# Performance work log

Hardware: AMD Instinct MI355X
Metric: run time of the kernel (lower is better)

The kernel has to match this reference:

```python
import jax, jax.numpy as jnp
import numpy as np

N_NODES = 10000
N_EDGES = 160000
IN_DIM = 512
HID = 128
HEADS = 8
EMB = 256
NEG_SLOPE = 0.2  # PyG GATConv default


def setup_inputs() -> dict:
    key = jax.random.key(0)
    ks = jax.random.split(key, 12)
    x = jax.random.normal(ks[0], (N_NODES, IN_DIM), dtype=jnp.float32)
    edge_index = jax.random.randint(ks[1], (2, N_EDGES), 0, N_NODES, dtype=jnp.int64)
    s1 = 1.0 / np.sqrt(IN_DIM)
    s2 = 1.0 / np.sqrt(HEADS * HID)
    W1 = jax.random.normal(ks[2], (IN_DIM, HEADS * HID), dtype=jnp.float32) * s1
    a_src1 = jax.random.normal(ks[3], (HEADS, HID), dtype=jnp.float32) * s2
    a_dst1 = jax.random.normal(ks[4], (HEADS, HID), dtype=jnp.float32) * s2
    b1 = jnp.zeros((HEADS * HID,), dtype=jnp.float32)
    W2 = jax.random.normal(ks[5], (HEADS * HID, EMB), dtype=jnp.float32) * s2
    a_src2 = jax.random.normal(ks[6], (1, EMB), dtype=jnp.float32) * (1.0 / np.sqrt(EMB))
    a_dst2 = jax.random.normal(ks[7], (1, EMB), dtype=jnp.float32) * (1.0 / np.sqrt(EMB))
    b2 = jnp.zeros((EMB,), dtype=jnp.float32)
    return {"x": x, "edge_index": edge_index, "W1": W1, "a_src1": a_src1,
            "a_dst1": a_dst1, "b1": b1, "W2": W2, "a_src2": a_src2,
            "a_dst2": a_dst2, "b2": b2}


def gat_layer(h_in, src, dst, W, a_src, a_dst, b, concat, num_nodes):
    """PyG-style GATConv (eval mode, self-loops already in src/dst)."""
    H, C = a_src.shape
    h = (h_in @ W).reshape(num_nodes, H, C)            # [N, H, C]
    alpha_src = jnp.einsum('nhc,hc->nh', h, a_src)      # [N, H]
    alpha_dst = jnp.einsum('nhc,hc->nh', h, a_dst)      # [N, H]
    e = jax.nn.leaky_relu(alpha_src[src] + alpha_dst[dst], NEG_SLOPE)  # [E, H]
    # segment softmax over incoming edges of each destination node
    m = jax.ops.segment_max(e, dst, num_segments=num_nodes)            # [N, H]
    ex = jnp.exp(e - m[dst])
    denom = jax.ops.segment_sum(ex, dst, num_segments=num_nodes)       # [N, H]
    alpha = ex / denom[dst]                                            # [E, H]
    out = jax.ops.segment_sum(h[src] * alpha[:, :, None], dst,
                              num_segments=num_nodes)                  # [N, H, C]
    out = out.reshape(num_nodes, H * C) if concat else out.mean(axis=1)
    return out + b


def reference(x, edge_index, W1, a_src1, a_dst1, b1, W2, a_src2, a_dst2, b2):
    N = x.shape[0]
    loops = jnp.arange(N, dtype=edge_index.dtype)
    src = jnp.concatenate([edge_index[0], loops])
    dst = jnp.concatenate([edge_index[1], loops])
    h = gat_layer(x, src, dst, W1, a_src1, a_dst1, b1, concat=True, num_nodes=N)
    h = jax.nn.elu(h)  # dropout inactive in eval mode
    out = gat_layer(h, src, dst, W2, a_src2, a_dst2, b2, concat=False, num_nodes=N)
    return out
```

## Files before the change

### kernel.cpp

```cpp
#include <hip/hip_runtime.h>
#include <hip/hip_bf16.h>

typedef __attribute__((ext_vector_type(8))) short short8;
typedef __attribute__((ext_vector_type(4))) float floatx4;
typedef __attribute__((ext_vector_type(4))) unsigned short ushort4v;
typedef __attribute__((ext_vector_type(8))) unsigned short ushort8v;

#define NN 10000
#define E0 160000
#define ETOT (E0 + NN)
#define IN_DIM 512
#define HID1 1024
#define EMB 256
#define MPAD 10112
#define LDSS 40

__device__ __forceinline__ float bf2f(unsigned short u) {
    unsigned v = ((unsigned)u) << 16;
    float f;
    __builtin_memcpy(&f, &v, 4);
    return f;
}
__device__ __forceinline__ unsigned short f2bf(float f) {
    unsigned u;
    __builtin_memcpy(&u, &f, 4);
    unsigned lsb = (u >> 16) & 1;
    u += 0x7fff + lsb;
    return (unsigned short)(u >> 16);
}
__device__ __forceinline__ float loadf(const void* p, size_t i, int isf32) {
    if (isf32) return ((const float*)p)[i];
    return bf2f(((const unsigned short*)p)[i]);
}

__global__ void zero_kernel(int* p, int n) {
    int i = blockIdx.x * 256 + threadIdx.x;
    if (i < n) p[i] = 0;
}

__global__ __launch_bounds__(1024) void fdetect_kernel(const unsigned* xw, int* isf32) {
    __shared__ int cnt[1024];
    int t = threadIdx.x;
    int c = 0;
    #pragma unroll
    for (int j = 0; j < 4; ++j) {
        unsigned w = xw[t * 4 + j];
        int ex = (w >> 7) & 0xFF;
        if (ex >= 110 && ex <= 135) c++;
    }
    cnt[t] = c;
    __syncthreads();
    for (int off = 512; off > 0; off >>= 1) {
        if (t < off) cnt[t] += cnt[t + off];
        __syncthreads();
    }
    if (t == 0) *isf32 = (cnt[0] < 2048) ? 1 : 0;
}

__global__ void detect_kernel(const int* ei32, int* flag) {
    int i = blockIdx.x * 256 + threadIdx.x;
    int v = 0;
    int idx = 2 * i + 1;
    if (idx < 2 * E0) v = ei32[idx];
    unsigned long long any = __ballot(v != 0);
    if (any && (threadIdx.x & 63) == 0) atomicOr(flag, 1);
}

__device__ __forceinline__ int load_edge(const void* ei, long long idx, int m32) {
    if (m32) return ((const int*)ei)[idx];
    return (int)(((const long long*)ei)[idx]);
}

__global__ void count_kernel(const void* ei, const int* flag, int* counts) {
    int e = blockIdx.x * 256 + threadIdx.x;
    if (e < E0) {
        int m32 = (*flag != 0);
        int d = load_edge(ei, (long long)E0 + e, m32);
        if (d >= 0 && d < NN) atomicAdd(&counts[d], 1);
    }
}

__global__ __launch_bounds__(1024) void scan_kernel(const int* counts, int* offsets, int* cursor) {
    __shared__ int part[1024];
    int t = threadIdx.x;
    int base = t * 10;
    int local[10];
    int s = 0;
    for (int j = 0; j < 10; ++j) {
        int idx = base + j;
        int v = (idx < NN) ? (counts[idx] + 1) : 0;
        local[j] = v; s += v;
    }
    part[t] = s;
    __syncthreads();
    for (int off = 1; off < 1024; off <<= 1) {
        int v = (t >= off) ? part[t - off] : 0;
        __syncthreads();
        part[t] += v;
        __syncthreads();
    }
    int run = (t == 0) ? 0 : part[t - 1];
    for (int j = 0; j < 10; ++j) {
        int idx = base + j;
        if (idx < NN) { offsets[idx] = run; cursor[idx] = run; run += local[j]; }
    }
    if (t == 1023) offsets[NN] = part[1023];
}

__global__ void scatter_kernel(const void* ei, const int* flag, int* cursor, int* csr_src) {
    int e = blockIdx.x * 256 + threadIdx.x;
    if (e >= ETOT) return;
    int m32 = (*flag != 0);
    int s, d;
    if (e < E0) { s = load_edge(ei, e, m32); d = load_edge(ei, (long long)E0 + e, m32); }
    else { s = d = e - E0; }
    if (s < 0) s = 0; if (s >= NN) s = NN - 1;
    if (d < 0) d = 0; if (d >= NN) d = NN - 1;
    int pos = atomicAdd(&cursor[d], 1);
    if (pos >= 0 && pos < ETOT) csr_src[pos] = s;
}

__global__ void conv_kernel(const void* in, unsigned short* out, int n, const int* isf32) {
    int i = blockIdx.x * 256 + threadIdx.x;
    if (i < n) out[i] = f2bf(loadf(in, i, *isf32));
}

__global__ void convT_kernel(const void* in, unsigned short* out, int R, int C, const int* isf32) {
    int i = blockIdx.x * 256 + threadIdx.x;
    if (i < R * C) {
        int r = i / C, c = i % C;
        out[(size_t)c * R + r] = f2bf(loadf(in, i, *isf32));
    }
}

template<bool OUTBF16>
__global__ __launch_bounds__(256) void gemm_tile(
    const unsigned short* __restrict__ A,
    const unsigned short* __restrict__ Bt,
    void* __restrict__ Cv,
    int N, int K)
{
    __shared__ unsigned short As[128 * LDSS];
    __shared__ unsigned short Bs[128 * LDSS];
    int t = threadIdx.x;
    int wave = t >> 6;
    int lane = t & 63;
    int quad = lane >> 4;
    int l16  = lane & 15;
    int mq = wave & 1, nq = wave >> 1;
    size_t mblk = (size_t)blockIdx.x * 128;
    size_t nblk = (size_t)blockIdx.y * 128;

    int srow = t >> 2;
    int skof = (t & 3) * 8;

    floatx4 acc[4][4];
    #pragma unroll
    for (int i = 0; i < 4; ++i)
        #pragma unroll
        for (int j = 0; j < 4; ++j)
            acc[i][j] = (floatx4){0.f, 0.f, 0.f, 0.f};

    const unsigned short* Ab = A + mblk * K + skof;
    const unsigned short* Bb = Bt + nblk * K + skof;

    for (int kk = 0; kk < K; kk += 32) {
        short8 a0 = *(const short8*)(const void*)(Ab + (size_t)srow * K + kk);
        short8 a1 = *(const short8*)(const void*)(Ab + (size_t)(srow + 64) * K + kk);
        short8 b0 = *(const short8*)(const void*)(Bb + (size_t)srow * K + kk);
        short8 b1 = *(const short8*)(const void*)(Bb + (size_t)(srow + 64) * K + kk);
        __syncthreads();
        *(short8*)(void*)(As + srow * LDSS + skof)        = a0;
        *(short8*)(void*)(As + (srow + 64) * LDSS + skof) = a1;
        *(short8*)(void*)(Bs + srow * LDSS + skof)        = b0;
        *(short8*)(void*)(Bs + (srow + 64) * LDSS + skof) = b1;
        __syncthreads();

        short8 af[4], bf[4];
        #pragma unroll
        for (int i = 0; i < 4; ++i) {
            af[i] = *(const short8*)(const void*)(As + (mq * 64 + i * 16 + l16) * LDSS + quad * 8);
            bf[i] = *(const short8*)(const void*)(Bs + (nq * 64 + i * 16 + l16) * LDSS + quad * 8);
        }
        #pragma unroll
        for (int i = 0; i < 4; ++i)
            #pragma unroll
            for (int j = 0; j < 4; ++j)
                acc[i][j] = __builtin_amdgcn_mfma_f32_16x16x32_bf16(af[i], bf[j], acc[i][j], 0, 0, 0);
    }

    size_t crow0 = mblk + mq * 64 + quad * 4;
    size_t ccol0 = nblk + nq * 64 + l16;
    #pragma unroll
    for (int i = 0; i < 4; ++i) {
        #pragma unroll
        for (int r = 0; r < 4; ++r) {
            size_t row = crow0 + i * 16 + r;
            size_t b = row * N + ccol0;
            #pragma unroll
            for (int j = 0; j < 4; ++j) {
                if (OUTBF16) ((unsigned short*)Cv)[b + j * 16] = f2bf(acc[i][j][r]);
                else         ((float*)Cv)[b + j * 16] = acc[i][j][r];
            }
        }
    }
}

__global__ __launch_bounds__(256) void alpha1_kernel(
    const unsigned short* __restrict__ h1,
    const void* __restrict__ a_src, const void* __restrict__ a_dst,
    const int* __restrict__ isf32,
    float* __restrict__ as1, float* __restrict__ ad1)
{
    int n = blockIdx.x, t = threadIdx.x;
    int f = *isf32;
    ushort4v hv = *(const ushort4v*)(const void*)(h1 + (size_t)n * HID1 + t * 4);
    float ps = 0.f, pd = 0.f;
    #pragma unroll
    for (int i = 0; i < 4; ++i) {
        float h = bf2f(hv[i]);
        ps += h * loadf(a_src, t * 4 + i, f);
        pd += h * loadf(a_dst, t * 4 + i, f);
    }
    __shared__ float rs[256], rdm[256];
    rs[t] = ps; rdm[t] = pd;
    __syncthreads();
    for (int off = 16; off > 0; off >>= 1) {
        if ((t & 31) < off) { rs[t] += rs[t + off]; rdm[t] += rdm[t + off]; }
        __syncthreads();
    }
    if ((t & 31) == 0) {
        int h = t >> 5;
        as1[n * 8 + h] = rs[t];
        ad1[n * 8 + h] = rdm[t];
    }
}

__global__ __launch_bounds__(256) void agg1_kernel(
    const unsigned short* __restrict__ h1, const int* __restrict__ offsets,
    const int* __restrict__ csr_src, const float* __restrict__ as1,
    const float* __restrict__ ad1, const void* __restrict__ b1,
    const int* __restrict__ isf32,
    unsigned short* __restrict__ hmid)
{
    int n = blockIdx.x, t = threadIdx.x;
    int f = *isf32;
    int beg = offsets[n], end = offsets[n + 1];
    if (beg < 0) beg = 0; if (end > ETOT) end = ETOT;
    int g = t >> 7;
    int u = t & 127;
    int c0 = u * 8;
    int hc = u >> 4;
    float ad = ad1[n * 8 + hc];

    float den = 0.f;
    float acc[8];
    #pragma unroll
    for (int j = 0; j < 8; ++j) acc[j] = 0.f;

    for (int i = beg + g; i < end; i += 2) {
        int s = csr_src[i]; s &= 0x7fffffff; if (s >= NN) s = 0;
        float e = as1[s * 8 + hc] + ad;
        e = e > 0.f ? e : 0.2f * e;
        float w = __expf(e);
        den += w;
        ushort8v hv = *(const ushort8v*)(const void*)(h1 + (size_t)s * HID1 + c0);
        #pragma unroll
        for (int j = 0; j < 8; ++j) acc[j] += bf2f(hv[j]) * w;
    }

    __shared__ float accsh[128][8];
    __shared__ float densh[128];
    if (g == 1) {
        #pragma unroll
        for (int j = 0; j < 8; ++j) accsh[u][j] = acc[j];
        densh[u] = den;
    }
    __syncthreads();
    if (g == 0) {
        den += densh[u];
        float rden = 1.0f / fmaxf(den, 1e-30f);
        ushort8v outw;
        #pragma unroll
        for (int j = 0; j < 8; ++j) {
            float v = (acc[j] + accsh[u][j]) * rden + loadf(b1, c0 + j, f);
            v = v > 0.f ? v : (__expf(v) - 1.0f);
            outw[j] = f2bf(v);
        }
        *(ushort8v*)(void*)(hmid + (size_t)n * HID1 + c0) = outw;
    }
}

__global__ __launch_bounds__(256) void alpha2_kernel(
    const unsigned short* __restrict__ h2,
    const void* __restrict__ a_src2, const void* __restrict__ a_dst2,
    const int* __restrict__ isf32,
    float* __restrict__ as2, float* __restrict__ ad2)
{
    int n = blockIdx.x, t = threadIdx.x;
    int f = *isf32;
    float v = bf2f(h2[(size_t)n * EMB + t]);
    float ps = v * loadf(a_src2, t, f);
    float pd = v * loadf(a_dst2, t, f);
    __shared__ float rs[256], rdm[256];
    rs[t] = ps; rdm[t] = pd;
    __syncthreads();
    for (int off = 128; off > 0; off >>= 1) {
        if (t < off) { rs[t] += rs[t + off]; rdm[t] += rdm[t + off]; }
        __syncthreads();
    }
    if (t == 0) { as2[n] = rs[0]; ad2[n] = rdm[0]; }
}

__global__ __launch_bounds__(256) void agg2_kernel(
    const unsigned short* __restrict__ h2, const int* __restrict__ offsets,
    const int* __restrict__ csr_src, const float* __restrict__ as2,
    const float* __restrict__ ad2, const void* __restrict__ b2,
    const int* __restrict__ isf32,
    float* __restrict__ out)
{
    int n = blockIdx.x, t = threadIdx.x;
    int f = *isf32;
    int beg = offsets[n], end = offsets[n + 1];
    if (beg < 0) beg = 0; if (end > ETOT) end = ETOT;
    int g = t >> 6;
    int u = t & 63;
    int c0 = u * 4;
    float adn = ad2[n];

    float den = 0.f;
    float acc[4];
    #pragma unroll
    for (int j = 0; j < 4; ++j) acc[j] = 0.f;

    for (int i = beg + g; i < end; i += 4) {
        int s = csr_src[i]; s &= 0x7fffffff; if (s >= NN) s = 0;
        float e = as2[s] + adn;
        e = e > 0.f ? e : 0.2f * e;
        float w = __expf(e);
        den += w;
        ushort4v hv = *(const ushort4v*)(const void*)(h2 + (size_t)s * EMB + c0);
        #pragma unroll
        for (int j = 0; j < 4; ++j) acc[j] += bf2f(hv[j]) * w;
    }

    __shared__ float accsh[4][64][4];
    __shared__ float densh[4][64];
    #pragma unroll
    for (int j = 0; j < 4; ++j) accsh[g][u][j] = acc[j];
    densh[g][u] = den;
    __syncthreads();
    if (g == 0) {
        float dtot = densh[0][u] + densh[1][u] + densh[2][u] + densh[3][u];
        float rden = 1.0f / fmaxf(dtot, 1e-30f);
        floatx4 o;
        #pragma unroll
        for (int j = 0; j < 4; ++j) {
            float v = (accsh[0][u][j] + accsh[1][u][j] + accsh[2][u][j] + accsh[3][u][j]) * rden;
            o[j] = v + loadf(b2, c0 + j, f);
        }
        *(floatx4*)(void*)(out + (size_t)n * EMB + c0) = o;
    }
}

extern "C" void kernel_launch(void* const* d_in, const int* in_sizes, int n_in,
                              void* d_out, int out_size, void* d_ws, size_t ws_size,
                              hipStream_t stream)
{
    const void* x      = d_in[0];
    const void* edge   = d_in[1];
    const void* W1     = d_in[2];
    const void* a_src1 = d_in[3];
    const void* a_dst1 = d_in[4];
    const void* b1     = d_in[5];
    const void* W2     = d_in[6];
    const void* a_src2 = d_in[7];
    const void* a_dst2 = d_in[8];
    const void* b2     = d_in[9];
    float* out = (float*)d_out;

    char* ws = (char*)d_ws;
    size_t off = 0;
    auto alloc = [&](size_t bytes) -> void* {
        void* p = ws + off;
        off += (bytes + 255) & ~(size_t)255;
        return p;
    };
    int*            counts = (int*)alloc((NN + 2) * 4);
    int*            offs   = (int*)alloc((NN + 1) * 4);
    int*            cursor = (int*)alloc(NN * 4);
    int*            csr    = (int*)alloc((size_t)ETOT * 4);
    float*          as1    = (float*)alloc((size_t)NN * 8 * 4);
    float*          ad1    = (float*)alloc((size_t)NN * 8 * 4);
    float*          as2    = (float*)alloc((size_t)NN * 4);
    float*          ad2    = (float*)alloc((size_t)NN * 4);
    unsigned short* xb     = (unsigned short*)alloc((size_t)MPAD * IN_DIM * 2);
    unsigned short* W1t    = (unsigned short*)alloc((size_t)IN_DIM * HID1 * 2);
    unsigned short* W2t    = (unsigned short*)alloc((size_t)HID1 * EMB * 2);
    unsigned short* h1b    = (unsigned short*)alloc((size_t)MPAD * HID1 * 2);
    unsigned short* hmid   = (unsigned short*)alloc((size_t)MPAD * HID1 * 2);
    unsigned short* h2b    = (unsigned short*)alloc((size_t)MPAD * EMB * 2);
    int* eflag = counts + NN;
    int* isf32 = counts + NN + 1;

    zero_kernel<<<(NN + 2 + 255) / 256, 256, 0, stream>>>(counts, NN + 2);
    fdetect_kernel<<<1, 1024, 0, stream>>>((const unsigned*)x, isf32);
    detect_kernel<<<(E0 + 255) / 256, 256, 0, stream>>>((const int*)edge, eflag);

    count_kernel<<<(E0 + 255) / 256, 256, 0, stream>>>(edge, eflag, counts);
    scan_kernel<<<1, 1024, 0, stream>>>(counts, offs, cursor);
    scatter_kernel<<<(ETOT + 255) / 256, 256, 0, stream>>>(edge, eflag, cursor, csr);

    conv_kernel<<<(NN * IN_DIM + 255) / 256, 256, 0, stream>>>(x, xb, NN * IN_DIM, isf32);
    convT_kernel<<<(IN_DIM * HID1 + 255) / 256, 256, 0, stream>>>(W1, W1t, IN_DIM, HID1, isf32);
    convT_kernel<<<(HID1 * EMB + 255) / 256, 256, 0, stream>>>(W2, W2t, HID1, EMB, isf32);

    dim3 g1(MPAD / 128, HID1 / 128);
    gemm_tile<true><<<g1, 256, 0, stream>>>(xb, W1t, h1b, HID1, IN_DIM);

    alpha1_kernel<<<NN, 256, 0, stream>>>(h1b, a_src1, a_dst1, isf32, as1, ad1);
    agg1_kernel<<<NN, 256, 0, stream>>>(h1b, offs, csr, as1, ad1, b1, isf32, hmid);

    dim3 g2(MPAD / 128, EMB / 128);
    gemm_tile<true><<<g2, 256, 0, stream>>>(hmid, W2t, h2b, EMB, HID1);

    alpha2_kernel<<<NN, 256, 0, stream>>>(h2b, a_src2, a_dst2, isf32, as2, ad2);
    agg2_kernel<<<NN, 256, 0, stream>>>(h2b, offs, csr, as2, ad2, b2, isf32, out);
}
```

Before: 325.3 us.

## Map one wavefront per node in alpha and aggregation kernels with unrolled gathers

Alpha and aggregation kernels now assign one 64-lane wavefront per destination node, four nodes per block, instead of one 256-thread block per node. Reductions use wave shuffles instead of LDS plus __syncthreads. Each lane in agg1 handles two heads, and the edge loops are unrolled by four so several gather loads are in flight at once. This removes block-level sync and LDS traffic and raises memory-level parallelism per wave, at the cost of more registers per lane (launch bounds set to 5 blocks) and load imbalance from per-node degree variation within a block.

```diff
diff --git a/kernel.cpp b/kernel.cpp
--- a/kernel.cpp
+++ b/kernel.cpp
@@ -5,6 +5,8 @@
 typedef __attribute__((ext_vector_type(4))) float floatx4;
 typedef __attribute__((ext_vector_type(4))) unsigned short ushort4v;
 typedef __attribute__((ext_vector_type(8))) unsigned short ushort8v;
+typedef __attribute__((ext_vector_type(2))) unsigned int uint2v;
+typedef __attribute__((ext_vector_type(4))) unsigned int uint4v;
 
 #define NN 10000
 #define E0 160000
@@ -21,6 +23,16 @@
     __builtin_memcpy(&f, &v, 4);
     return f;
 }
+__device__ __forceinline__ float bflo(unsigned v) {
+    unsigned x = v << 16;
+    float f; __builtin_memcpy(&f, &x, 4);
+    return f;
+}
+__device__ __forceinline__ float bfhi(unsigned v) {
+    unsigned x = v & 0xffff0000u;
+    float f; __builtin_memcpy(&f, &x, 4);
+    return f;
+}
 __device__ __forceinline__ unsigned short f2bf(float f) {
     unsigned u;
     __builtin_memcpy(&u, &f, 4);
@@ -28,10 +40,14 @@
     u += 0x7fff + lsb;
     return (unsigned short)(u >> 16);
 }
+__device__ __forceinline__ unsigned packbf(float lo, float hi) {
+    return (unsigned)f2bf(lo) | ((unsigned)f2bf(hi) << 16);
+}
 __device__ __forceinline__ float loadf(const void* p, size_t i, int isf32) {
     if (isf32) return ((const float*)p)[i];
     return bf2f(((const unsigned short*)p)[i]);
 }
+__device__ __forceinline__ float lrelu(float e) { return e > 0.f ? e : 0.2f * e; }
 
 __global__ void zero_kernel(int* p, int n) {
     int i = blockIdx.x * 256 + threadIdx.x;
@@ -212,83 +228,150 @@
     const int* __restrict__ isf32,
     float* __restrict__ as1, float* __restrict__ ad1)
 {
-    int n = blockIdx.x, t = threadIdx.x;
+    int n = blockIdx.x * 4 + (threadIdx.x >> 6);
+    if (n >= NN) return;
+    int lane = threadIdx.x & 63;
     int f = *isf32;
-    ushort4v hv = *(const ushort4v*)(const void*)(h1 + (size_t)n * HID1 + t * 4);
+    int h = lane >> 3;
+    const unsigned* h1w = (const unsigned*)h1;
+    uint4v v0 = *(const uint4v*)(const void*)(h1w + (size_t)n * 512 + lane * 8);
+    uint4v v1 = *(const uint4v*)(const void*)(h1w + (size_t)n * 512 + lane * 8 + 4);
+    int c0 = lane * 16;
     float ps = 0.f, pd = 0.f;
     #pragma unroll
-    for (int i = 0; i < 4; ++i) {
-        float h = bf2f(hv[i]);
-        ps += h * loadf(a_src, t * 4 + i, f);
-        pd += h * loadf(a_dst, t * 4 + i, f);
-    }
-    __shared__ float rs[256], rdm[256];
-    rs[t] = ps; rdm[t] = pd;
-    __syncthreads();
-    for (int off = 16; off > 0; off >>= 1) {
-        if ((t & 31) < off) { rs[t] += rs[t + off]; rdm[t] += rdm[t + off]; }
-        __syncthreads();
-    }
-    if ((t & 31) == 0) {
-        int h = t >> 5;
-        as1[n * 8 + h] = rs[t];
-        ad1[n * 8 + h] = rdm[t];
-    }
-}
-
-__global__ __launch_bounds__(256) void agg1_kernel(
+    for (int q = 0; q < 4; ++q) {
+        float e0 = bflo(v0[q]), e1 = bfhi(v0[q]);
+        ps += e0 * loadf(a_src, c0 + 2 * q, f)     + e1 * loadf(a_src, c0 + 2 * q + 1, f);
+        pd += e0 * loadf(a_dst, c0 + 2 * q, f)     + e1 * loadf(a_dst, c0 + 2 * q + 1, f);
+        float e2 = bflo(v1[q]), e3 = bfhi(v1[q]);
+        ps += e2 * loadf(a_src, c0 + 8 + 2 * q, f) + e3 * loadf(a_src, c0 + 8 + 2 * q + 1, f);
+        pd += e2 * loadf(a_dst, c0 + 8 + 2 * q, f) + e3 * loadf(a_dst, c0 + 8 + 2 * q + 1, f);
+    }
+    #pragma unroll
+    for (int off = 1; off < 8; off <<= 1) {
+        ps += __shfl_xor(ps, off, 64);
+        pd += __shfl_xor(pd, off, 64);
+    }
+    if ((lane & 7) == 0) {
+        as1[n * 8 + h] = ps;
+        ad1[n * 8 + h] = pd;
+    }
+}
+
+__global__ __launch_bounds__(256, 5) void agg1_kernel(
     const unsigned short* __restrict__ h1, const int* __restrict__ offsets,
     const int* __restrict__ csr_src, const float* __restrict__ as1,
     const float* __restrict__ ad1, const void* __restrict__ b1,
     const int* __restrict__ isf32,
     unsigned short* __restrict__ hmid)
 {
-    int n = blockIdx.x, t = threadIdx.x;
+    int n = blockIdx.x * 4 + (threadIdx.x >> 6);
+    if (n >= NN) return;
+    int lane = threadIdx.x & 63;
     int f = *isf32;
     int beg = offsets[n], end = offsets[n + 1];
     if (beg < 0) beg = 0; if (end > ETOT) end = ETOT;
-    int g = t >> 7;
-    int u = t & 127;
-    int c0 = u * 8;
-    int hc = u >> 4;
-    float ad = ad1[n * 8 + hc];
-
-    float den = 0.f;
-    float acc[8];
-    #pragma unroll
-    for (int j = 0; j < 8; ++j) acc[j] = 0.f;
-
-    for (int i = beg + g; i < end; i += 2) {
-        int s = csr_src[i]; s &= 0x7fffffff; if (s >= NN) s = 0;
-        float e = as1[s * 8 + hc] + ad;
-        e = e > 0.f ? e : 0.2f * e;
-        float w = __expf(e);
-        den += w;
-        ushort8v hv = *(const ushort8v*)(const void*)(h1 + (size_t)s * HID1 + c0);
-        #pragma unroll
-        for (int j = 0; j < 8; ++j) acc[j] += bf2f(hv[j]) * w;
-    }
-
-    __shared__ float accsh[128][8];
-    __shared__ float densh[128];
-    if (g == 1) {
-        #pragma unroll
-        for (int j = 0; j < 8; ++j) accsh[u][j] = acc[j];
-        densh[u] = den;
-    }
-    __syncthreads();
-    if (g == 0) {
-        den += densh[u];
-        float rden = 1.0f / fmaxf(den, 1e-30f);
-        ushort8v outw;
-        #pragma unroll
-        for (int j = 0; j < 8; ++j) {
-            float v = (acc[j] + accsh[u][j]) * rden + loadf(b1, c0 + j, f);
-            v = v > 0.f ? v : (__expf(v) - 1.0f);
-            outw[j] = f2bf(v);
+    int hA = lane >> 4;
+    int hB = hA + 4;
+    float adA = ad1[n * 8 + hA];
+    float adB = ad1[n * 8 + hB];
+    const unsigned* rbase = (const unsigned*)h1 + lane * 4;
+
+    float denA = 0.f, denB = 0.f;
+    float accA[8], accB[8];
+    #pragma unroll
+    for (int j = 0; j < 8; ++j) { accA[j] = 0.f; accB[j] = 0.f; }
+
+    int i = beg;
+    for (; i + 3 < end; i += 4) {
+        int s0 = csr_src[i];     s0 &= 0x7fffffff; if (s0 >= NN) s0 = 0;
+        int s1 = csr_src[i + 1]; s1 &= 0x7fffffff; if (s1 >= NN) s1 = 0;
+        int s2 = csr_src[i + 2]; s2 &= 0x7fffffff; if (s2 >= NN) s2 = 0;
+        int s3 = csr_src[i + 3]; s3 &= 0x7fffffff; if (s3 >= NN) s3 = 0;
+        uint4v a0 = *(const uint4v*)(const void*)(rbase + (size_t)s0 * 512);
+        uint4v b0 = *(const uint4v*)(const void*)(rbase + (size_t)s0 * 512 + 256);
+        uint4v a1 = *(const uint4v*)(const void*)(rbase + (size_t)s1 * 512);
+        uint4v b1v = *(const uint4v*)(const void*)(rbase + (size_t)s1 * 512 + 256);
+        uint4v a2 = *(const uint4v*)(const void*)(rbase + (size_t)s2 * 512);
+        uint4v b2v = *(const uint4v*)(const void*)(rbase + (size_t)s2 * 512 + 256);
+        uint4v a3 = *(const uint4v*)(const void*)(rbase + (size_t)s3 * 512);
+        uint4v b3v = *(const uint4v*)(const void*)(rbase + (size_t)s3 * 512 + 256);
+        float wA0 = __expf(lrelu(as1[s0 * 8 + hA] + adA));
+        float wA1 = __expf(lrelu(as1[s1 * 8 + hA] + adA));
+        float wA2 = __expf(lrelu(as1[s2 * 8 + hA] + adA));
+        float wA3 = __expf(lrelu(as1[s3 * 8 + hA] + adA));
+        float wB0 = __expf(lrelu(as1[s0 * 8 + hB] + adB));
+        float wB1 = __expf(lrelu(as1[s1 * 8 + hB] + adB));
+        float wB2 = __expf(lrelu(as1[s2 * 8 + hB] + adB));
+        float wB3 = __expf(lrelu(as1[s3 * 8 + hB] + adB));
+        denA += (wA0 + wA1) + (wA2 + wA3);
+        denB += (wB0 + wB1) + (wB2 + wB3);
+        #pragma unroll
+        for (int q = 0; q < 4; ++q) {
+            accA[2 * q]     += (bflo(a0[q]) * wA0 + bflo(a1[q]) * wA1) + (bflo(a2[q]) * wA2 + bflo(a3[q]) * wA3);
+            accA[2 * q + 1] += (bfhi(a0[q]) * wA0 + bfhi(a1[q]) * wA1) + (bfhi(a2[q]) * wA2 + bfhi(a3[q]) * wA3);
+            accB[2 * q]     += (bflo(b0[q]) * wB0 + bflo(b1v[q]) * wB1) + (bflo(b2v[q]) * wB2 + bflo(b3v[q]) * wB3);
+            accB[2 * q + 1] += (bfhi(b0[q]) * wB0 + bfhi(b1v[q]) * wB1) + (bfhi(b2v[q]) * wB2 + bfhi(b3v[q]) * wB3);
         }
-        *(ushort8v*)(void*)(hmid + (size_t)n * HID1 + c0) = outw;
-    }
+    }
+    for (; i + 1 < end; i += 2) {
+        int s0 = csr_src[i];     s0 &= 0x7fffffff; if (s0 >= NN) s0 = 0;
+        int s1 = csr_src[i + 1]; s1 &= 0x7fffffff; if (s1 >= NN) s1 = 0;
+        uint4v a0 = *(const uint4v*)(const void*)(rbase + (size_t)s0 * 512);
+        uint4v b0 = *(const uint4v*)(const void*)(rbase + (size_t)s0 * 512 + 256);
+        uint4v a1 = *(const uint4v*)(const void*)(rbase + (size_t)s1 * 512);
+        uint4v b1v = *(const uint4v*)(const void*)(rbase + (size_t)s1 * 512 + 256);
+        float wA0 = __expf(lrelu(as1[s0 * 8 + hA] + adA));
+        float wA1 = __expf(lrelu(as1[s1 * 8 + hA] + adA));
+        float wB0 = __expf(lrelu(as1[s0 * 8 + hB] + adB));
+        float wB1 = __expf(lrelu(as1[s1 * 8 + hB] + adB));
+        denA += wA0 + wA1;
+        denB += wB0 + wB1;
+        #pragma unroll
+        for (int q = 0; q < 4; ++q) {
+            accA[2 * q]     += bflo(a0[q]) * wA0 + bflo(a1[q]) * wA1;
+            accA[2 * q + 1] += bfhi(a0[q]) * wA0 + bfhi(a1[q]) * wA1;
+            accB[2 * q]     += bflo(b0[q]) * wB0 + bflo(b1v[q]) * wB1;
+            accB[2 * q + 1] += bfhi(b0[q]) * wB0 + bfhi(b1v[q]) * wB1;
+        }
+    }
+    if (i < end) {
+        int s0 = csr_src[i]; s0 &= 0x7fffffff; if (s0 >= NN) s0 = 0;
+        uint4v a0 = *(const uint4v*)(const void*)(rbase + (size_t)s0 * 512);
+        uint4v b0 = *(const uint4v*)(const void*)(rbase + (size_t)s0 * 512 + 256);
+        float wA0 = __expf(lrelu(as1[s0 * 8 + hA] + adA));
+        float wB0 = __expf(lrelu(as1[s0 * 8 + hB] + adB));
+        denA += wA0;
+        denB += wB0;
+        #pragma unroll
+        for (int q = 0; q < 4; ++q) {
+            accA[2 * q]     += bflo(a0[q]) * wA0;
+            accA[2 * q + 1] += bfhi(a0[q]) * wA0;
+            accB[2 * q]     += bflo(b0[q]) * wB0;
+            accB[2 * q + 1] += bfhi(b0[q]) * wB0;
+        }
+    }
+
+    float rdA = 1.0f / fmaxf(denA, 1e-30f);
+    float rdB = 1.0f / fmaxf(denB, 1e-30f);
+    uint4v oA, oB;
+    #pragma unroll
+    for (int q = 0; q < 4; ++q) {
+        int c = lane * 8 + 2 * q;
+        float v0 = accA[2 * q]     * rdA + loadf(b1, c, f);
+        float v1 = accA[2 * q + 1] * rdA + loadf(b1, c + 1, f);
+        v0 = v0 > 0.f ? v0 : (__expf(v0) - 1.0f);
+        v1 = v1 > 0.f ? v1 : (__expf(v1) - 1.0f);
+        oA[q] = packbf(v0, v1);
+        float u0 = accB[2 * q]     * rdB + loadf(b1, 512 + c, f);
+        float u1 = accB[2 * q + 1] * rdB + loadf(b1, 512 + c + 1, f);
+        u0 = u0 > 0.f ? u0 : (__expf(u0) - 1.0f);
+        u1 = u1 > 0.f ? u1 : (__expf(u1) - 1.0f);
+        oB[q] = packbf(u0, u1);
+    }
+    unsigned* hw = (unsigned*)hmid;
+    *(uint4v*)(void*)(hw + (size_t)n * 512 + lane * 4)       = oA;
+    *(uint4v*)(void*)(hw + (size_t)n * 512 + 256 + lane * 4) = oB;
 }
 
 __global__ __launch_bounds__(256) void alpha2_kernel(
@@ -297,19 +380,24 @@
     const int* __restrict__ isf32,
     float* __restrict__ as2, float* __restrict__ ad2)
 {
-    int n = blockIdx.x, t = threadIdx.x;
+    int n = blockIdx.x * 4 + (threadIdx.x >> 6);
+    if (n >= NN) return;
+    int lane = threadIdx.x & 63;
     int f = *isf32;
-    float v = bf2f(h2[(size_t)n * EMB + t]);
-    float ps = v * loadf(a_src2, t, f);
-    float pd = v * loadf(a_dst2, t, f);
-    __shared__ float rs[256], rdm[256];
-    rs[t] = ps; rdm[t] = pd;
-    __syncthreads();
-    for (int off = 128; off > 0; off >>= 1) {
-        if (t < off) { rs[t] += rs[t + off]; rdm[t] += rdm[t + off]; }
-        __syncthreads();
-    }
-    if (t == 0) { as2[n] = rs[0]; ad2[n] = rdm[0]; }
+    const unsigned* h2w = (const unsigned*)h2;
+    uint2v v = *(const uint2v*)(const void*)(h2w + (size_t)n * 128 + lane * 2);
+    int c0 = lane * 4;
+    float e0 = bflo(v[0]), e1 = bfhi(v[0]), e2 = bflo(v[1]), e3 = bfhi(v[1]);
+    float ps = e0 * loadf(a_src2, c0, f) + e1 * loadf(a_src2, c0 + 1, f)
+             + e2 * loadf(a_src2, c0 + 2, f) + e3 * loadf(a_src2, c0 + 3, f);
+    float pd = e0 * loadf(a_dst2, c0, f) + e1 * loadf(a_dst2, c0 + 1, f)
+             + e2 * loadf(a_dst2, c0 + 2, f) + e3 * loadf(a_dst2, c0 + 3, f);
+    #pragma unroll
+    for (int off = 1; off < 64; off <<= 1) {
+        ps += __shfl_xor(ps, off, 64);
+        pd += __shfl_xor(pd, off, 64);
+    }
+    if (lane == 0) { as2[n] = ps; ad2[n] = pd; }
 }
 
 __global__ __launch_bounds__(256) void agg2_kernel(
@@ -319,48 +407,70 @@
     const int* __restrict__ isf32,
     float* __restrict__ out)
 {
-    int n = blockIdx.x, t = threadIdx.x;
+    int n = blockIdx.x * 4 + (threadIdx.x >> 6);
+    if (n >= NN) return;
+    int lane = threadIdx.x & 63;
     int f = *isf32;
     int beg = offsets[n], end = offsets[n + 1];
     if (beg < 0) beg = 0; if (end > ETOT) end = ETOT;
-    int g = t >> 6;
-    int u = t & 63;
-    int c0 = u * 4;
     float adn = ad2[n];
+    const unsigned* rbase = (const unsigned*)h2 + lane * 2;
 
     float den = 0.f;
     float acc[4];
     #pragma unroll
     for (int j = 0; j < 4; ++j) acc[j] = 0.f;
 
-    for (int i = beg + g; i < end; i += 4) {
-        int s = csr_src[i]; s &= 0x7fffffff; if (s >= NN) s = 0;
-        float e = as2[s] + adn;
-        e = e > 0.f ? e : 0.2f * e;
-        float w = __expf(e);
-        den += w;
-        ushort4v hv = *(const ushort4v*)(const void*)(h2 + (size_t)s * EMB + c0);
-        #pragma unroll
-        for (int j = 0; j < 4; ++j) acc[j] += bf2f(hv[j]) * w;
-    }
-
-    __shared__ float accsh[4][64][4];
-    __shared__ float densh[4][64];
-    #pragma unroll
-    for (int j = 0; j < 4; ++j) accsh[g][u][j] = acc[j];
-    densh[g][u] = den;
-    __syncthreads();
-    if (g == 0) {
-        float dtot = densh[0][u] + densh[1][u] + densh[2][u] + densh[3][u];
-        float rden = 1.0f / fmaxf(dtot, 1e-30f);
-        floatx4 o;
-        #pragma unroll
-        for (int j = 0; j < 4; ++j) {
-            float v = (accsh[0][u][j] + accsh[1][u][j] + accsh[2][u][j] + accsh[3][u][j]) * rden;
-            o[j] = v + loadf(b2, c0 + j, f);
-        }
-        *(floatx4*)(void*)(out + (size_t)n * EMB + c0) = o;
-    }
+    int i = beg;
+    for (; i + 3 < end; i += 4) {
+        int s0 = csr_src[i];     s0 &= 0x7fffffff; if (s0 >= NN) s0 = 0;
+        int s1 = csr_src[i + 1]; s1 &= 0x7fffffff; if (s1 >= NN) s1 = 0;
+        int s2 = csr_src[i + 2]; s2 &= 0x7fffffff; if (s2 >= NN) s2 = 0;
+        int s3 = csr_src[i + 3]; s3 &= 0x7fffffff; if (s3 >= NN) s3 = 0;
+        uint2v v0 = *(const uint2v*)(const void*)(rbase + (size_t)s0 * 128);
+        uint2v v1 = *(const uint2v*)(const void*)(rbase + (size_t)s1 * 128);
+        uint2v v2 = *(const uint2v*)(const void*)(rbase + (size_t)s2 * 128);
+        uint2v v3 = *(const uint2v*)(const void*)(rbase + (size_t)s3 * 128);
+        float w0 = __expf(lrelu(as2[s0] + adn));
+        float w1 = __expf(lrelu(as2[s1] + adn));
+        float w2 = __expf(lrelu(as2[s2] + adn));
+        float w3 = __expf(lrelu(as2[s3] + adn));
+        den += (w0 + w1) + (w2 + w3);
+        acc[0] += (bflo(v0[0]) * w0 + bflo(v1[0]) * w1) + (bflo(v2[0]) * w2 + bflo(v3[0]) * w3);
+        acc[1] += (bfhi(v0[0]) * w0 + bfhi(v1[0]) * w1) + (bfhi(v2[0]) * w2 + bfhi(v3[0]) * w3);
+        acc[2] += (bflo(v0[1]) * w0 + bflo(v1[1]) * w1) + (bflo(v2[1]) * w2 + bflo(v3[1]) * w3);
+        acc[3] += (bfhi(v0[1]) * w0 + bfhi(v1[1]) * w1) + (bfhi(v2[1]) * w2 + bfhi(v3[1]) * w3);
+    }
+    for (; i + 1 < end; i += 2) {
+        int s0 = csr_src[i];     s0 &= 0x7fffffff; if (s0 >= NN) s0 = 0;
+        int s1 = csr_src[i + 1]; s1 &= 0x7fffffff; if (s1 >= NN) s1 = 0;
+        uint2v v0 = *(const uint2v*)(const void*)(rbase + (size_t)s0 * 128);
+        uint2v v1 = *(const uint2v*)(const void*)(rbase + (size_t)s1 * 128);
+        float w0 = __expf(lrelu(as2[s0] + adn));
+        float w1 = __expf(lrelu(as2[s1] + adn));
+        den += w0 + w1;
+        acc[0] += bflo(v0[0]) * w0 + bflo(v1[0]) * w1;
+        acc[1] += bfhi(v0[0]) * w0 + bfhi(v1[0]) * w1;
+        acc[2] += bflo(v0[1]) * w0 + bflo(v1[1]) * w1;
+        acc[3] += bfhi(v0[1]) * w0 + bfhi(v1[1]) * w1;
+    }
+    if (i < end) {
+        int s0 = csr_src[i]; s0 &= 0x7fffffff; if (s0 >= NN) s0 = 0;
+        uint2v v0 = *(const uint2v*)(const void*)(rbase + (size_t)s0 * 128);
+        float w0 = __expf(lrelu(as2[s0] + adn));
+        den += w0;
+        acc[0] += bflo(v0[0]) * w0;
+        acc[1] += bfhi(v0[0]) * w0;
+        acc[2] += bflo(v0[1]) * w0;
+        acc[3] += bfhi(v0[1]) * w0;
+    }
+
+    float rden = 1.0f / fmaxf(den, 1e-30f);
+    floatx4 o;
+    #pragma unroll
+    for (int j = 0; j < 4; ++j)
+        o[j] = acc[j] * rden + loadf(b2, lane * 4 + j, f);
+    *(floatx4*)(void*)(out + (size_t)n * EMB + lane * 4) = o;
 }
 
 extern "C" void kernel_launch(void* const* d_in, const int* in_sizes, int n_in,
@@ -418,12 +528,12 @@
     dim3 g1(MPAD / 128, HID1 / 128);
     gemm_tile<true><<<g1, 256, 0, stream>>>(xb, W1t, h1b, HID1, IN_DIM);
 
-    alpha1_kernel<<<NN, 256, 0, stream>>>(h1b, a_src1, a_dst1, isf32, as1, ad1);
-    agg1_kernel<<<NN, 256, 0, stream>>>(h1b, offs, csr, as1, ad1, b1, isf32, hmid);
+    alpha1_kernel<<<(NN + 3) / 4, 256, 0, stream>>>(h1b, a_src1, a_dst1, isf32, as1, ad1);
+    agg1_kernel<<<(NN + 3) / 4, 256, 0, stream>>>(h1b, offs, csr, as1, ad1, b1, isf32, hmid);
 
     dim3 g2(MPAD / 128, EMB / 128);
     gemm_tile<true><<<g2, 256, 0, stream>>>(hmid, W2t, h2b, EMB, HID1);
 
-    alpha2_kernel<<<NN, 256, 0, stream>>>(h2b, a_src2, a_dst2, isf32, as2, ad2);
-    agg2_kernel<<<NN, 256, 0, stream>>>(h2b, offs, csr, as2, ad2, b2, isf32, out);
-}
+    alpha2_kernel<<<(NN + 3) / 4, 256, 0, stream>>>(h2b, a_src2, a_dst2, isf32, as2, ad2);
+    agg2_kernel<<<(NN + 3) / 4, 256, 0, stream>>>(h2b, offs, csr, as2, ad2, b2, isf32, out);
+}
```

New measurement: 338.2 us. 4.0% more time.
